# Optimization experiments

Hardware: AMD Instinct MI355X
Metric: run time of the kernel (lower is better)

## Reference

```python
import jax, jax.numpy as jnp
import numpy as np

B, N, C, O, K, D = 32, 2048, 64, 64, 3, 16

def setup_inputs() -> dict:
    key = jax.random.key(0)
    ks = jax.random.split(key, 6)
    x = jax.random.normal(ks[0], (B, N, C), dtype=jnp.float32)
    node_embeddings = jax.random.normal(ks[1], (N, D), dtype=jnp.float32)
    adj_m = jax.random.uniform(ks[2], (N, N), dtype=jnp.float32)
    weights_pool = jax.random.normal(ks[3], (D, K, C, O), dtype=jnp.float32) * 0.1
    bias_pool = jax.random.normal(ks[4], (D, O), dtype=jnp.float32) * 0.1
    sa_weight = jax.random.normal(ks[5], (N, 2 * N), dtype=jnp.float32) * (1.0 / np.sqrt(2 * N))
    return {"x": x, "node_embeddings": node_embeddings, "adj_m": adj_m,
            "weights_pool": weights_pool, "bias_pool": bias_pool, "sa_weight": sa_weight}

def reference(x, node_embeddings, adj_m, weights_pool, bias_pool, sa_weight):
    n = node_embeddings.shape[0]
    # learned adaptive adjacency [N,N]
    supports = jax.nn.softmax(jax.nn.relu(node_embeddings @ node_embeddings.T), axis=1)
    # SpatialAttention: 1x1 conv over 2N channels == matmul with [N,2N] weight
    z = jnp.concatenate([supports, adj_m], axis=1) @ sa_weight.T  # [N,N]
    s2 = jax.nn.sigmoid(z)
    supports = s2 * adj_m + (1.0 - s2) * supports
    # Chebyshev polynomial basis
    support_set = [jnp.eye(n, dtype=supports.dtype), supports]
    for _ in range(2, K):
        support_set.append(2.0 * supports @ support_set[-1] - support_set[-2])
    supports_k = jnp.stack(support_set, axis=0)  # [K,N,N]
    # per-node generated weights/bias from embeddings
    weights = jnp.einsum('nd,dkio->nkio', node_embeddings, weights_pool)  # [N,K,C,O]
    bias = node_embeddings @ bias_pool  # [N,O]
    # graph conv: aggregate then per-node matmul
    x_g = jnp.einsum('knm,bmc->bnkc', supports_k, x)  # [B,N,K,C]
    x_gconv = jnp.einsum('bnki,nkio->bno', x_g, weights) + bias  # [B,N,O]
    return x_gconv
```

## Files before the change

### kernel.cpp

```cpp
#include <hip/hip_runtime.h>


typedef unsigned short u16;
typedef float f32x4 __attribute__((ext_vector_type(4)));
typedef __bf16 bf16x8 __attribute__((ext_vector_type(8)));
typedef unsigned short u16x8 __attribute__((ext_vector_type(8)));

#define PSTRIDE ((size_t)2048 * 2048)

__device__ __forceinline__ u16 f2bf(float f) {
    unsigned u = __float_as_uint(f);
    u += 0x7FFFu + ((u >> 16) & 1u);
    return (u16)(u >> 16);
}
__device__ __forceinline__ float bf2f(u16 h) {
    return __uint_as_float((unsigned)h << 16);
}
__device__ __forceinline__ void gl_lds16(const void* g, void* l) {
    __builtin_amdgcn_global_load_lds(
        (const __attribute__((address_space(1))) unsigned*)g,
        (__attribute__((address_space(3))) unsigned*)l, 16, 0, 0);
}

__global__ __launch_bounds__(256)
void preamble(const float* __restrict__ E, const float* __restrict__ adj,
              const float* __restrict__ saw, const float* __restrict__ x,
              const float* __restrict__ Wp, const float* __restrict__ bp,
              float* __restrict__ zf, u16* __restrict__ Acat,
              u16* __restrict__ sawb, u16* __restrict__ xtT,
              u16* __restrict__ Wpb, float* __restrict__ Wpbf,
              float* __restrict__ bias, u16* __restrict__ xn, int mode) {
    __shared__ u16 t[64][65];
    __shared__ float Bp[1024];
    const int bid = blockIdx.x, tid = threadIdx.x;

    if (bid < 256) {
        const int c0 = (bid & 31) * 64, r0 = (bid >> 5) * 256;
        const int r = r0 + tid;
        const float4* Er = (const float4*)(E + (size_t)r * 16);
        float4 e0 = Er[0], e1 = Er[1], e2 = Er[2], e3 = Er[3];
        *(float4*)(Bp + tid * 4) = *(const float4*)(E + (size_t)c0 * 16 + tid * 4);
        __syncthreads();
        float* zr = zf + (size_t)r * 2048 + c0;
#pragma unroll
        for (int cc = 0; cc < 4; ++cc) {
            float acc[16];
#pragma unroll
            for (int c = 0; c < 16; ++c) {
                const float* bp2 = Bp + (cc * 16 + c) * 16;
                float s = 0.f;
                s = fmaf(e0.x, bp2[0], s);  s = fmaf(e0.y, bp2[1], s);
                s = fmaf(e0.z, bp2[2], s);  s = fmaf(e0.w, bp2[3], s);
                s = fmaf(e1.x, bp2[4], s);  s = fmaf(e1.y, bp2[5], s);
                s = fmaf(e1.z, bp2[6], s);  s = fmaf(e1.w, bp2[7], s);
                s = fmaf(e2.x, bp2[8], s);  s = fmaf(e2.y, bp2[9], s);
                s = fmaf(e2.z, bp2[10], s); s = fmaf(e2.w, bp2[11], s);
                s = fmaf(e3.x, bp2[12], s); s = fmaf(e3.y, bp2[13], s);
                s = fmaf(e3.z, bp2[14], s); s = fmaf(e3.w, bp2[15], s);
                acc[c] = fmaxf(s, 0.f);
            }
#pragma unroll
            for (int q = 0; q < 4; ++q)
                *(float4*)(zr + cc * 16 + q * 4) =
                    make_float4(acc[q * 4], acc[q * 4 + 1], acc[q * 4 + 2], acc[q * 4 + 3]);
        }
    } else if (bid < 4352) {
        size_t j = ((size_t)(bid - 256) * 256 + tid) * 4;
        float4 v = *(const float4*)(adj + j);
        int n = (int)(j >> 11), c = (int)(j & 2047);
        ushort4 o = make_ushort4(f2bf(v.x), f2bf(v.y), f2bf(v.z), f2bf(v.w));
        *(ushort4*)(Acat + (size_t)n * 4096 + 2048 + c) = o;
    } else if (bid < 12544) {
        size_t j = ((size_t)(bid - 4352) * 256 + tid) * 4;
        float4 v = *(const float4*)(saw + j);
        ushort4 o = make_ushort4(f2bf(v.x), f2bf(v.y), f2bf(v.z), f2bf(v.w));
        *(ushort4*)(sawb + j) = o;
    } else if (bid < 13568) {
        int local = bid - 12544;
        int m0 = (local & 31) * 64, b = local >> 5;
        int c = tid & 63, g = tid >> 6;
#pragma unroll
        for (int r = 0; r < 16; ++r) {
            int mm = g * 16 + r;
            t[mm][c] = f2bf(x[((size_t)b * 2048 + m0 + mm) * 64 + c]);
        }
        __syncthreads();
#pragma unroll
        for (int r = 0; r < 16; ++r) {
            int cc = g * 16 + r;
            xtT[((size_t)b * 64 + cc) * 2048 + m0 + c] = t[c][cc];
        }
        if (mode) {
#pragma unroll
            for (int r = 0; r < 16; ++r) {
                int mm = g * 16 + r;
                xn[((size_t)(m0 + mm)) * 2048 + b * 64 + c] = t[mm][c];
            }
        }
    } else {
        int local = bid - 13568;
        if (local < 16) {
            const int d = local;
            const float* base = Wp + (size_t)d * 12288;
            for (int idx = tid; idx < 12288; idx += 256) {
                int o = idx / 192, ki = idx - o * 192;
                int k = ki >> 6, i = ki & 63;
                float v;
                if (k == 0)      v = base[i * 64 + o] - base[2 * 4096 + i * 64 + o];
                else if (k == 1) v = base[4096 + i * 64 + o];
                else             v = 2.f * base[2 * 4096 + i * 64 + o];
                size_t dst = (size_t)(d * 64 + o) * 192 + ki;
                Wpb[dst] = f2bf(v);
                Wpbf[dst] = v;
            }
        } else {
            const int nb = local - 16;
#pragma unroll
            for (int it = 0; it < 8; ++it) {
                int idx = tid + it * 256;
                int n = nb * 32 + (idx >> 6), o = idx & 63;
                float s = 0.f;
#pragma unroll
                for (int d = 0; d < 16; ++d) s = fmaf(E[n * 16 + d], bp[d * 64 + o], s);
                bias[(size_t)n * 64 + o] = s;
            }
        }
    }
}

__global__ __launch_bounds__(256)
void mid(const float* __restrict__ zf, u16* __restrict__ Acat,
         const float* __restrict__ E, const float* __restrict__ Wpbf,
         u16* __restrict__ Wnb) {
    __shared__ float red[4];
    __shared__ float Es[32 * 16];
    const int bid = blockIdx.x, tid = threadIdx.x;
    if (bid < 2048) {
        const int n = bid, lane = tid & 63, wave = tid >> 6;
        const float* zr = zf + (size_t)n * 2048;
        float4 a = *(const float4*)(zr + tid * 8);
        float4 b = *(const float4*)(zr + tid * 8 + 4);
        float mx = fmaxf(fmaxf(fmaxf(a.x, a.y), fmaxf(a.z, a.w)),
                         fmaxf(fmaxf(b.x, b.y), fmaxf(b.z, b.w)));
        for (int off = 32; off; off >>= 1) mx = fmaxf(mx, __shfl_down(mx, off, 64));
        if (lane == 0) red[wave] = mx;
        __syncthreads();
        mx = fmaxf(fmaxf(red[0], red[1]), fmaxf(red[2], red[3]));
        __syncthreads();
        float v[8] = {__expf(a.x - mx), __expf(a.y - mx), __expf(a.z - mx), __expf(a.w - mx),
                      __expf(b.x - mx), __expf(b.y - mx), __expf(b.z - mx), __expf(b.w - mx)};
        float sum = v[0] + v[1] + v[2] + v[3] + v[4] + v[5] + v[6] + v[7];
        for (int off = 32; off; off >>= 1) sum += __shfl_down(sum, off, 64);
        if (lane == 0) red[wave] = sum;
        __syncthreads();
        sum = red[0] + red[1] + red[2] + red[3];
        float inv = 1.f / sum;
        u16* orow = Acat + (size_t)n * 4096 + tid * 8;
        *(ushort4*)orow = make_ushort4(f2bf(v[0] * inv), f2bf(v[1] * inv),
                                       f2bf(v[2] * inv), f2bf(v[3] * inv));
        *(ushort4*)(orow + 4) = make_ushort4(f2bf(v[4] * inv), f2bf(v[5] * inv),
                                             f2bf(v[6] * inv), f2bf(v[7] * inv));
    } else {
        const int w = bid - 2048;
        const int c0 = (w % 12) * 1024, n0 = (w / 12) * 32;
        for (int j = tid; j < 512; j += 256) Es[j] = E[(size_t)n0 * 16 + j];
        float4 wf[16];
#pragma unroll
        for (int d = 0; d < 16; ++d)
            wf[d] = *(const float4*)(Wpbf + (size_t)d * 12288 + c0 + tid * 4);
        __syncthreads();
        for (int nl = 0; nl < 32; ++nl) {
            float4 s = make_float4(0.f, 0.f, 0.f, 0.f);
#pragma unroll
            for (int d = 0; d < 16; ++d) {
                float e = Es[nl * 16 + d];
                s.x = fmaf(e, wf[d].x, s.x);
                s.y = fmaf(e, wf[d].y, s.y);
                s.z = fmaf(e, wf[d].z, s.z);
                s.w = fmaf(e, wf[d].w, s.w);
            }
            *(ushort4*)(Wnb + (size_t)(n0 + nl) * 12288 + c0 + tid * 4) =
                make_ushort4(f2bf(s.x), f2bf(s.y), f2bf(s.z), f2bf(s.w));
        }
    }
}

__global__ __launch_bounds__(256, 3)
void gemm_bt(const u16* __restrict__ A, const u16* __restrict__ Bt,
             u16* __restrict__ Cp, int M, int N, int K, int Kh) {
    __shared__ alignas(16) u16 As[128 * 64];
    __shared__ alignas(16) u16 Bs[128 * 64];
    const int tid = threadIdx.x, lane = tid & 63, wave = tid >> 6;
    const int m0 = blockIdx.y * 128, n0 = blockIdx.x * 128;
    const int wm = (wave >> 1) * 64, wn = (wave & 1) * 64;
    const int kbeg = blockIdx.z * Kh, kend = kbeg + Kh;
    const int ml = lane & 15, c0l = lane >> 4;
    f32x4 acc[4][4] = {};

    int sIdx[4], rowI[4], gcI[4];
#pragma unroll
    for (int r = 0; r < 4; ++r) {
        int s = wave * 64 + r * 256 + lane;
        sIdx[r] = s; rowI[r] = s >> 3; gcI[r] = (s & 7) ^ ((s >> 3) & 7);
    }
    int baseA[4], mskA[4], baseB[4], mskB[4];
#pragma unroll
    for (int i = 0; i < 4; ++i) { int m = wm + i * 16 + ml; baseA[i] = m * 8; mskA[i] = m & 7; }
#pragma unroll
    for (int j = 0; j < 4; ++j) { int nn = wn + j * 16 + ml; baseB[j] = nn * 8; mskB[j] = nn & 7; }

    u16x8 ra[4], rb[4];
#pragma unroll
    for (int r = 0; r < 4; ++r) {
        ra[r] = *(const u16x8*)(A + (size_t)(m0 + rowI[r]) * K + kbeg + gcI[r] * 8);
        rb[r] = *(const u16x8*)(Bt + (size_t)(n0 + rowI[r]) * K + kbeg + gcI[r] * 8);
    }
#pragma unroll
    for (int r = 0; r < 4; ++r) {
        *(u16x8*)(As + (size_t)sIdx[r] * 8) = ra[r];
        *(u16x8*)(Bs + (size_t)sIdx[r] * 8) = rb[r];
    }
    __syncthreads();

    for (int k0 = kbeg; k0 < kend; k0 += 64) {
        const bool more = (k0 + 64) < kend;
        if (more) {
#pragma unroll
            for (int r = 0; r < 4; ++r) {
                ra[r] = *(const u16x8*)(A + (size_t)(m0 + rowI[r]) * K + (k0 + 64) + gcI[r] * 8);
                rb[r] = *(const u16x8*)(Bt + (size_t)(n0 + rowI[r]) * K + (k0 + 64) + gcI[r] * 8);
            }
        }
#pragma unroll
        for (int ks4 = 0; ks4 < 8; ks4 += 4) {
            bf16x8 af[4], bv[4];
#pragma unroll
            for (int i = 0; i < 4; ++i)
                af[i] = *(const bf16x8*)(As + (baseA[i] + ((c0l + ks4) ^ mskA[i])) * 8);
#pragma unroll
            for (int j = 0; j < 4; ++j)
                bv[j] = *(const bf16x8*)(Bs + (baseB[j] + ((c0l + ks4) ^ mskB[j])) * 8);
#pragma unroll
            for (int i = 0; i < 4; ++i)
#pragma unroll
                for (int j = 0; j < 4; ++j)
                    acc[i][j] = __builtin_amdgcn_mfma_f32_16x16x32_bf16(af[i], bv[j], acc[i][j], 0, 0, 0);
        }
        if (more) {
            __syncthreads();
#pragma unroll
            for (int r = 0; r < 4; ++r) {
                *(u16x8*)(As + (size_t)sIdx[r] * 8) = ra[r];
                *(u16x8*)(Bs + (size_t)sIdx[r] * 8) = rb[r];
            }
            __syncthreads();
        }
    }

    const int col_l = lane & 15, row_l = (lane >> 4) * 4;
    u16* Cz = Cp + (size_t)blockIdx.z * M * N;
#pragma unroll
    for (int i = 0; i < 4; ++i)
#pragma unroll
        for (int j = 0; j < 4; ++j)
#pragma unroll
            for (int r = 0; r < 4; ++r) {
                int row = m0 + wm + i * 16 + row_l + r;
                int col = n0 + wn + j * 16 + col_l;
                Cz[(size_t)row * N + col] = f2bf(acc[i][j][r]);
            }
}

__global__ __launch_bounds__(256)
void reduce_z(const u16* __restrict__ p, const u16* __restrict__ Acat,
              u16* __restrict__ S) {
    size_t j = ((size_t)blockIdx.x * 256 + threadIdx.x) * 4;
    ushort4 p0 = *(const ushort4*)(p + j);
    ushort4 p1 = *(const ushort4*)(p + PSTRIDE + j);
    ushort4 p2 = *(const ushort4*)(p + 2 * PSTRIDE + j);
    ushort4 p3 = *(const ushort4*)(p + 3 * PSTRIDE + j);
    int row = (int)(j >> 11), col = (int)(j & 2047);
    ushort4 sp = *(const ushort4*)(Acat + (size_t)row * 4096 + col);
    ushort4 ad = *(const ushort4*)(Acat + (size_t)row * 4096 + 2048 + col);
    float z0 = bf2f(p0.x) + bf2f(p1.x) + bf2f(p2.x) + bf2f(p3.x);
    float z1 = bf2f(p0.y) + bf2f(p1.y) + bf2f(p2.y) + bf2f(p3.y);
    float z2 = bf2f(p0.z) + bf2f(p1.z) + bf2f(p2.z) + bf2f(p3.z);
    float z3 = bf2f(p0.w) + bf2f(p1.w) + bf2f(p2.w) + bf2f(p3.w);
    float s0 = 1.f / (1.f + __expf(-z0)), s1 = 1.f / (1.f + __expf(-z1));
    float s2 = 1.f / (1.f + __expf(-z2)), s3 = 1.f / (1.f + __expf(-z3));
    ushort4 o = make_ushort4(
        f2bf(s0 * bf2f(ad.x) + (1.f - s0) * bf2f(sp.x)),
        f2bf(s1 * bf2f(ad.y) + (1.f - s1) * bf2f(sp.y)),
        f2bf(s2 * bf2f(ad.z) + (1.f - s2) * bf2f(sp.z)),
        f2bf(s3 * bf2f(ad.w) + (1.f - s3) * bf2f(sp.w)));
    *(ushort4*)(S + j) = o;
}

__global__ __launch_bounds__(256)
void reduceT(const u16* __restrict__ p, u16* __restrict__ xg1o,
             u16* __restrict__ xg1T, int mode) {
    __shared__ u16 t[64][68];
    int bx = blockIdx.x * 64, by = blockIdx.y * 64;
    int cg = threadIdx.x & 15, rg = threadIdx.x >> 4;
    int b = bx >> 6;
#pragma unroll
    for (int rr = 0; rr < 4; ++rr) {
        int row = rg * 4 + rr;
        size_t idx = (size_t)(by + row) * 2048 + bx + cg * 4;
        ushort4 q0 = *(const ushort4*)(p + idx);
        ushort4 q1 = *(const ushort4*)(p + PSTRIDE + idx);
        ushort4 q2 = *(const ushort4*)(p + 2 * PSTRIDE + idx);
        ushort4 q3 = *(const ushort4*)(p + 3 * PSTRIDE + idx);
        ushort4 v = make_ushort4(
            f2bf(bf2f(q0.x) + bf2f(q1.x) + bf2f(q2.x) + bf2f(q3.x)),
            f2bf(bf2f(q0.y) + bf2f(q1.y) + bf2f(q2.y) + bf2f(q3.y)),
            f2bf(bf2f(q0.z) + bf2f(q1.z) + bf2f(q2.z) + bf2f(q3.z)),
            f2bf(bf2f(q0.w) + bf2f(q1.w) + bf2f(q2.w) + bf2f(q3.w)));
        if (mode) *(ushort4*)(xg1o + idx) = v;
        else      *(ushort4*)(xg1o + ((size_t)b * 2048 + by + row) * 64 + cg * 4) = v;
        *(ushort4*)(&t[row][cg * 4]) = v;
    }
    __syncthreads();
    int c = threadIdx.x & 63, g = threadIdx.x >> 6;
#pragma unroll
    for (int r = 0; r < 16; ++r) {
        int row = g * 16 + r;
        xg1T[(size_t)(bx + row) * 2048 + by + c] = t[c][row];
    }
}

__global__ __launch_bounds__(256, 4)
void gconv_wn(const u16* __restrict__ xn, const u16* __restrict__ xg1n,
              const u16* __restrict__ p, const u16* __restrict__ Wnb,
              const float* __restrict__ bias, float* __restrict__ out) {
    __shared__ alignas(16) u16 As[32 * 192];
    __shared__ alignas(16) u16 Bs[64 * 192];
    const int n = blockIdx.x, tid = threadIdx.x;
    const int lane = tid & 63, wave = tid >> 6;
    const int wn2 = wave * 16;
    const int ml = lane & 15, c0l = lane >> 4;
    const int col = lane & 15, rl = (lane >> 4) * 4;

#pragma unroll
    for (int it = 0; it < 6; ++it) {
        int s = tid + it * 256;
        int row = s / 24, sc = s - row * 24;
        int gc = (sc & 24) | ((sc ^ row) & 7);
        gl_lds16(Wnb + (size_t)n * 12288 + (size_t)row * 192 + gc * 8, Bs + (size_t)s * 8);
    }
#pragma unroll
    for (int it = 0; it < 3; ++it) {
        int s = tid + it * 256;
        int row = s / 24, sc = s - row * 24;
        int gc = (sc & 24) | ((sc ^ row) & 7);
        u16x8 v;
        if (gc < 8) {
            v = *(const u16x8*)(xn + (size_t)n * 2048 + row * 64 + (gc & 7) * 8);
        } else if (gc < 16) {
            v = *(const u16x8*)(xg1n + (size_t)n * 2048 + row * 64 + (gc & 7) * 8);
        } else {
            const u16* pp = p + (size_t)n * 2048 + row * 64 + (gc & 7) * 8;
            u16x8 q0 = *(const u16x8*)pp;
            u16x8 q1 = *(const u16x8*)(pp + PSTRIDE);
            u16x8 q2 = *(const u16x8*)(pp + 2 * PSTRIDE);
            u16x8 q3 = *(const u16x8*)(pp + 3 * PSTRIDE);
#pragma unroll
            for (int tt = 0; tt < 8; ++tt)
                v[tt] = f2bf(bf2f(q0[tt]) + bf2f(q1[tt]) + bf2f(q2[tt]) + bf2f(q3[tt]));
        }
        *(u16x8*)(As + (size_t)s * 8) = v;
    }
    float bv0 = bias[(size_t)n * 64 + wn2 + col];
    f32x4 acc[2];
#pragma unroll
    for (int mt = 0; mt < 2; ++mt)
#pragma unroll
        for (int r = 0; r < 4; ++r) acc[mt][r] = bv0;
    __syncthreads();

#pragma unroll
    for (int ks = 0; ks < 6; ++ks) {
        int c = c0l + ks * 4;
        int o = wn2 + ml;
        bf16x8 bfrag = *(const bf16x8*)(Bs + (o * 24 + ((c & 24) | ((c ^ (o & 7)) & 7))) * 8);
#pragma unroll
        for (int mt = 0; mt < 2; ++mt) {
            int m = mt * 16 + ml;
            bf16x8 afrag = *(const bf16x8*)(As + (m * 24 + ((c & 24) | ((c ^ (m & 7)) & 7))) * 8);
            acc[mt] = __builtin_amdgcn_mfma_f32_16x16x32_bf16(afrag, bfrag, acc[mt], 0, 0, 0);
        }
    }
#pragma unroll
    for (int mt = 0; mt < 2; ++mt)
#pragma unroll
        for (int r = 0; r < 4; ++r) {
            int b = mt * 16 + rl + r;
            out[((size_t)b * 2048 + n) * 64 + wn2 + col] = acc[mt][r];
        }
}

__global__ __launch_bounds__(256, 2)
void gconv_mfma(const float* __restrict__ x, const u16* __restrict__ xg1,
                const u16* __restrict__ p, const u16* __restrict__ Wpb,
                const float* __restrict__ bias, const float* __restrict__ E,
                float* __restrict__ out) {
    __shared__ alignas(16) float El[16 * 128];
    const int tid = threadIdx.x, lane = tid & 63, wave = tid >> 6;
    const int m0 = blockIdx.x * 128, nb = m0 & 2047, bB = m0 >> 11;
    const int wm = (wave >> 1) * 64, wn = (wave & 1) * 32;
    const int ml = lane & 15, c0l = lane >> 4;
    const int col_l = lane & 15, rl = (lane >> 4) * 4;

#pragma unroll
    for (int it = 0; it < 8; ++it) {
        int idx = tid + it * 256;
        El[idx] = E[(size_t)(nb + (idx & 127)) * 16 + (idx >> 7)];
    }
    __syncthreads();

    bf16x8 af[4][6];
#pragma unroll
    for (int i = 0; i < 4; ++i) {
        const int row = m0 + wm + i * 16 + ml;
        const int n = row & 2047;
#pragma unroll
        for (int ks = 0; ks < 2; ++ks) {
            const float* xp = x + (size_t)row * 64 + (c0l + ks * 4) * 8;
            float4 a = *(const float4*)xp, b4 = *(const float4*)(xp + 4);
            u16x8 v;
            v[0] = f2bf(a.x);  v[1] = f2bf(a.y);  v[2] = f2bf(a.z);  v[3] = f2bf(a.w);
            v[4] = f2bf(b4.x); v[5] = f2bf(b4.y); v[6] = f2bf(b4.z); v[7] = f2bf(b4.w);
            af[i][ks] = __builtin_bit_cast(bf16x8, v);
        }
#pragma unroll
        for (int ks = 2; ks < 4; ++ks)
            af[i][ks] = *(const bf16x8*)(xg1 + (size_t)row * 64 + (c0l + ks * 4 - 8) * 8);
#pragma unroll
        for (int ks = 4; ks < 6; ++ks) {
            const u16* pp = p + (size_t)n * 2048 + bB * 64 + (c0l + ks * 4 - 16) * 8;
            u16x8 q0 = *(const u16x8*)pp;
            u16x8 q1 = *(const u16x8*)(pp + PSTRIDE);
            u16x8 q2 = *(const u16x8*)(pp + 2 * PSTRIDE);
            u16x8 q3 = *(const u16x8*)(pp + 3 * PSTRIDE);
            u16x8 v;
#pragma unroll
            for (int tt = 0; tt < 8; ++tt)
                v[tt] = f2bf(bf2f(q0[tt]) + bf2f(q1[tt]) + bf2f(q2[tt]) + bf2f(q3[tt]));
            af[i][ks] = __builtin_bit_cast(bf16x8, v);
        }
    }

    f32x4 oacc[4][2];
#pragma unroll
    for (int i = 0; i < 4; ++i)
#pragma unroll
        for (int j = 0; j < 2; ++j)
#pragma unroll
            for (int r = 0; r < 4; ++r)
                oacc[i][j][r] = bias[(size_t)(nb + wm + i * 16 + rl + r) * 64 + wn + j * 16 + col_l];

#pragma unroll 2
    for (int d = 0; d < 16; ++d) {
        bf16x8 bv[2][6];
#pragma unroll
        for (int j = 0; j < 2; ++j) {
            const u16* wp = Wpb + (size_t)(d * 64 + wn + j * 16 + ml) * 192 + c0l * 8;
#pragma unroll
            for (int ks = 0; ks < 6; ++ks)
                bv[j][ks] = *(const bf16x8*)(wp + ks * 32);
        }
        f32x4 tmp[4][2] = {};
#pragma unroll
        for (int ks = 0; ks < 6; ++ks)
#pragma unroll
            for (int i = 0; i < 4; ++i)
#pragma unroll
                for (int j = 0; j < 2; ++j)
                    tmp[i][j] = __builtin_amdgcn_mfma_f32_16x16x32_bf16(af[i][ks], bv[j][ks], tmp[i][j], 0, 0, 0);
#pragma unroll
        for (int i = 0; i < 4; ++i) {
            f32x4 ev = *(const f32x4*)(El + d * 128 + wm + i * 16 + rl);
#pragma unroll
            for (int r = 0; r < 4; ++r)
#pragma unroll
                for (int j = 0; j < 2; ++j)
                    oacc[i][j][r] = fmaf(ev[r], tmp[i][j][r], oacc[i][j][r]);
        }
    }
#pragma unroll
    for (int i = 0; i < 4; ++i)
#pragma unroll
        for (int j = 0; j < 2; ++j)
#pragma unroll
            for (int r = 0; r < 4; ++r)
                out[(size_t)(m0 + wm + i * 16 + rl + r) * 64 + wn + j * 16 + col_l] = oacc[i][j][r];
}

extern "C" void kernel_launch(void* const* d_in, const int* in_sizes, int n_in,
                              void* d_out, int out_size, void* d_ws, size_t ws_size,
                              hipStream_t stream) {
    const float* x   = (const float*)d_in[0];
    const float* E   = (const float*)d_in[1];
    const float* adj = (const float*)d_in[2];
    const float* Wp  = (const float*)d_in[3];
    const float* bp  = (const float*)d_in[4];
    const float* saw = (const float*)d_in[5];
    float* out = (float*)d_out;

    char* ws = (char*)d_ws;
    const size_t MB = 1u << 20;
    const int wn_mode = (ws_size >= 140 * MB) ? 1 : 0;

    u16*   Acat  = (u16*)(ws);
    u16*   sawb  = (u16*)(ws + 16 * MB);
    u16*   XtT   = (u16*)(ws + 32 * MB);
    u16*   Wpb   = (u16*)(ws + 40 * MB);
    float* bias  = (float*)(ws + 41 * MB);
    float* Wpbf  = (float*)(ws + 42 * MB);
    float* zf    = (float*)(ws + 48 * MB);
    u16*   part  = (u16*)(ws + 48 * MB);
    u16*   S_bf  = (u16*)(ws + 16 * MB);
    u16*   xg1T  = (u16*)(ws + 24 * MB);
    u16*   xg1o  = (u16*)(ws);
    u16*   xn    = (u16*)(ws + 80 * MB);
    u16*   Wnb   = (u16*)(ws + 88 * MB);

    preamble<<<13648, 256, 0, stream>>>(E, adj, saw, x, Wp, bp, zf, Acat, sawb, XtT,
                                        Wpb, Wpbf, bias, xn, wn_mode);
    mid<<<wn_mode ? 2816 : 2048, 256, 0, stream>>>(zf, Acat, E, Wpbf, Wnb);

    gemm_bt<<<dim3(16, 16, 4), 256, 0, stream>>>(Acat, sawb, part, 2048, 2048, 4096, 1024);
    reduce_z<<<4096, 256, 0, stream>>>(part, Acat, S_bf);
    gemm_bt<<<dim3(16, 16, 4), 256, 0, stream>>>(S_bf, XtT, part, 2048, 2048, 2048, 512);
    reduceT<<<dim3(32, 32), 256, 0, stream>>>(part, xg1o, xg1T, wn_mode);
    gemm_bt<<<dim3(16, 16, 4), 256, 0, stream>>>(S_bf, xg1T, part, 2048, 2048, 2048, 512);

    if (wn_mode)
        gconv_wn<<<2048, 256, 0, stream>>>(xn, xg1o, part, Wnb, bias, out);
    else
        gconv_mfma<<<512, 256, 0, stream>>>(x, xg1o, part, Wpb, bias, E, out);
}
```

Before: 278.6 us.

## Replace GEMM with 256x256 tile, double-buffered direct-to-LDS loads and XCD remap

The bf16 MFMA GEMM moves from 128x128 tiles with 256 threads to 256x256 tiles with 512 threads and 8 waves. Global data now goes straight into LDS through global_load_lds into a double buffer, so the next K-slice loads while the current one is computed. MFMA bursts are split into four quadrant phases with barriers and s_setprio, and workgroup IDs are remapped so blocks spread across XCDs. Each GEMM now launches only 256 workgroups with 128KB of LDS per block, which may underfill the GPU's 256 CUs and limits how many blocks fit per CU.

```diff
diff --git a/kernel.cpp b/kernel.cpp
--- a/kernel.cpp
+++ b/kernel.cpp
@@ -185,87 +185,162 @@
     }
 }
 
-__global__ __launch_bounds__(256, 3)
-void gemm_bt(const u16* __restrict__ A, const u16* __restrict__ Bt,
-             u16* __restrict__ Cp, int M, int N, int K, int Kh) {
-    __shared__ alignas(16) u16 As[128 * 64];
-    __shared__ alignas(16) u16 Bs[128 * 64];
+__global__ __launch_bounds__(512, 2)
+void gemm_bt256(const u16* __restrict__ A, const u16* __restrict__ Bt,
+                u16* __restrict__ Cp, int M, int N, int K, int Kh) {
+    __shared__ alignas(16) u16 As[2][256 * 64];
+    __shared__ alignas(16) u16 Bs[2][256 * 64];
     const int tid = threadIdx.x, lane = tid & 63, wave = tid >> 6;
-    const int m0 = blockIdx.y * 128, n0 = blockIdx.x * 128;
-    const int wm = (wave >> 1) * 64, wn = (wave & 1) * 64;
-    const int kbeg = blockIdx.z * Kh, kend = kbeg + Kh;
+
+    const int nbx = gridDim.x, nby = gridDim.y, nbz = gridDim.z;
+    const int nwg = nbx * nby * nbz;
+    int lin = (blockIdx.z * nby + blockIdx.y) * nbx + blockIdx.x;
+    if ((nwg & 7) == 0) lin = (lin & 7) * (nwg >> 3) + (lin >> 3);
+    const int bz = lin / (nbx * nby);
+    const int r2 = lin - bz * nbx * nby;
+    const int by = r2 / nbx, bx = r2 - by * nbx;
+
+    const int m0 = by * 256, n0 = bx * 256;
+    const int kbeg = bz * Kh;
+    const int NT = Kh >> 6;
+    const int wm = (wave >> 2) * 128, wn = (wave & 3) * 64;
     const int ml = lane & 15, c0l = lane >> 4;
-    f32x4 acc[4][4] = {};
-
-    int sIdx[4], rowI[4], gcI[4];
+
+    int sI[4], rowI[4], gcI[4];
 #pragma unroll
     for (int r = 0; r < 4; ++r) {
-        int s = wave * 64 + r * 256 + lane;
-        sIdx[r] = s; rowI[r] = s >> 3; gcI[r] = (s & 7) ^ ((s >> 3) & 7);
-    }
-    int baseA[4], mskA[4], baseB[4], mskB[4];
-#pragma unroll
-    for (int i = 0; i < 4; ++i) { int m = wm + i * 16 + ml; baseA[i] = m * 8; mskA[i] = m & 7; }
-#pragma unroll
-    for (int j = 0; j < 4; ++j) { int nn = wn + j * 16 + ml; baseB[j] = nn * 8; mskB[j] = nn & 7; }
-
-    u16x8 ra[4], rb[4];
-#pragma unroll
-    for (int r = 0; r < 4; ++r) {
-        ra[r] = *(const u16x8*)(A + (size_t)(m0 + rowI[r]) * K + kbeg + gcI[r] * 8);
-        rb[r] = *(const u16x8*)(Bt + (size_t)(n0 + rowI[r]) * K + kbeg + gcI[r] * 8);
-    }
-#pragma unroll
-    for (int r = 0; r < 4; ++r) {
-        *(u16x8*)(As + (size_t)sIdx[r] * 8) = ra[r];
-        *(u16x8*)(Bs + (size_t)sIdx[r] * 8) = rb[r];
-    }
-    __syncthreads();
-
-    for (int k0 = kbeg; k0 < kend; k0 += 64) {
-        const bool more = (k0 + 64) < kend;
-        if (more) {
+        int s = r * 512 + tid;
+        sI[r] = s; rowI[r] = s >> 3; gcI[r] = (s & 7) ^ ((s >> 3) & 7);
+    }
+
+    f32x4 acc[8][4] = {};
+
+#pragma unroll
+    for (int r = 0; r < 4; ++r)
+        gl_lds16(A + (size_t)(m0 + rowI[r]) * K + kbeg + gcI[r] * 8, &As[0][sI[r] * 8]);
+#pragma unroll
+    for (int r = 0; r < 4; ++r)
+        gl_lds16(Bt + (size_t)(n0 + rowI[r]) * K + kbeg + gcI[r] * 8, &Bs[0][sI[r] * 8]);
+    asm volatile("s_waitcnt vmcnt(0)" ::: "memory");
+    __builtin_amdgcn_s_barrier();
+
+    for (int t = 0; t < NT; ++t) {
+        const int cur = t & 1;
+        const u16* Asc = As[cur];
+        const u16* Bsc = Bs[cur];
+
+        if (t + 1 < NT) {
+            const int k1 = kbeg + (t + 1) * 64;
+            u16* Ad = (u16*)As[cur ^ 1];
+            u16* Bd = (u16*)Bs[cur ^ 1];
+#pragma unroll
+            for (int r = 0; r < 4; ++r)
+                gl_lds16(A + (size_t)(m0 + rowI[r]) * K + k1 + gcI[r] * 8, Ad + sI[r] * 8);
+#pragma unroll
+            for (int r = 0; r < 4; ++r)
+                gl_lds16(Bt + (size_t)(n0 + rowI[r]) * K + k1 + gcI[r] * 8, Bd + sI[r] * 8);
+        }
+
+        bf16x8 af[4][2], bv[2][2];
+
+#pragma unroll
+        for (int i = 0; i < 4; ++i) {
+            const int mr = wm + i * 16 + ml;
+#pragma unroll
+            for (int ks = 0; ks < 2; ++ks)
+                af[i][ks] = *(const bf16x8*)(Asc + mr * 64 + (((c0l + ks * 4) ^ (mr & 7)) * 8));
+        }
+#pragma unroll
+        for (int j = 0; j < 2; ++j) {
+            const int nr = wn + j * 16 + ml;
+#pragma unroll
+            for (int ks = 0; ks < 2; ++ks)
+                bv[j][ks] = *(const bf16x8*)(Bsc + nr * 64 + (((c0l + ks * 4) ^ (nr & 7)) * 8));
+        }
+        __builtin_amdgcn_s_barrier();
+        asm volatile("s_waitcnt lgkmcnt(0)" ::: "memory");
+        __builtin_amdgcn_s_setprio(1);
+#pragma unroll
+        for (int ks = 0; ks < 2; ++ks)
+#pragma unroll
+            for (int i = 0; i < 4; ++i)
+#pragma unroll
+                for (int j = 0; j < 2; ++j)
+                    acc[i][j] = __builtin_amdgcn_mfma_f32_16x16x32_bf16(af[i][ks], bv[j][ks], acc[i][j], 0, 0, 0);
+        __builtin_amdgcn_s_setprio(0);
+        __builtin_amdgcn_s_barrier();
+
+#pragma unroll
+        for (int j = 0; j < 2; ++j) {
+            const int nr = wn + (2 + j) * 16 + ml;
+#pragma unroll
+            for (int ks = 0; ks < 2; ++ks)
+                bv[j][ks] = *(const bf16x8*)(Bsc + nr * 64 + (((c0l + ks * 4) ^ (nr & 7)) * 8));
+        }
+        __builtin_amdgcn_s_barrier();
+        asm volatile("s_waitcnt lgkmcnt(0)" ::: "memory");
+        __builtin_amdgcn_s_setprio(1);
+#pragma unroll
+        for (int ks = 0; ks < 2; ++ks)
+#pragma unroll
+            for (int i = 0; i < 4; ++i)
+#pragma unroll
+                for (int j = 0; j < 2; ++j)
+                    acc[i][2 + j] = __builtin_amdgcn_mfma_f32_16x16x32_bf16(af[i][ks], bv[j][ks], acc[i][2 + j], 0, 0, 0);
+        __builtin_amdgcn_s_setprio(0);
+        __builtin_amdgcn_s_barrier();
+
+#pragma unroll
+        for (int i = 0; i < 4; ++i) {
+            const int mr = wm + (4 + i) * 16 + ml;
+#pragma unroll
+            for (int ks = 0; ks < 2; ++ks)
+                af[i][ks] = *(const bf16x8*)(Asc + mr * 64 + (((c0l + ks * 4) ^ (mr & 7)) * 8));
+        }
+        __builtin_amdgcn_s_barrier();
+        asm volatile("s_waitcnt lgkmcnt(0)" ::: "memory");
+        __builtin_amdgcn_s_setprio(1);
+#pragma unroll
+        for (int ks = 0; ks < 2; ++ks)
+#pragma unroll
+            for (int i = 0; i < 4; ++i)
+#pragma unroll
+                for (int j = 0; j < 2; ++j)
+                    acc[4 + i][2 + j] = __builtin_amdgcn_mfma_f32_16x16x32_bf16(af[i][ks], bv[j][ks], acc[4 + i][2 + j], 0, 0, 0);
+        __builtin_amdgcn_s_setprio(0);
+        __builtin_amdgcn_s_barrier();
+
+#pragma unroll
+        for (int j = 0; j < 2; ++j) {
+            const int nr = wn + j * 16 + ml;
+#pragma unroll
+            for (int ks = 0; ks < 2; ++ks)
+                bv[j][ks] = *(const bf16x8*)(Bsc + nr * 64 + (((c0l + ks * 4) ^ (nr & 7)) * 8));
+        }
+        __builtin_amdgcn_s_barrier();
+        asm volatile("s_waitcnt lgkmcnt(0)" ::: "memory");
+        __builtin_amdgcn_s_setprio(1);
+#pragma unroll
+        for (int ks = 0; ks < 2; ++ks)
+#pragma unroll
+            for (int i = 0; i < 4; ++i)
+#pragma unroll
+                for (int j = 0; j < 2; ++j)
+                    acc[4 + i][j] = __builtin_amdgcn_mfma_f32_16x16x32_bf16(af[i][ks], bv[j][ks], acc[4 + i][j], 0, 0, 0);
+        __builtin_amdgcn_s_setprio(0);
+        asm volatile("s_waitcnt vmcnt(0)" ::: "memory");
+        __builtin_amdgcn_s_barrier();
+    }
+
+    const int col_l = lane & 15, rl = (lane >> 4) * 4;
+    u16* Cz = Cp + (size_t)bz * M * N;
+#pragma unroll
+    for (int i = 0; i < 8; ++i)
+#pragma unroll
+        for (int j = 0; j < 4; ++j)
 #pragma unroll
             for (int r = 0; r < 4; ++r) {
-                ra[r] = *(const u16x8*)(A + (size_t)(m0 + rowI[r]) * K + (k0 + 64) + gcI[r] * 8);
-                rb[r] = *(const u16x8*)(Bt + (size_t)(n0 + rowI[r]) * K + (k0 + 64) + gcI[r] * 8);
-            }
-        }
-#pragma unroll
-        for (int ks4 = 0; ks4 < 8; ks4 += 4) {
-            bf16x8 af[4], bv[4];
-#pragma unroll
-            for (int i = 0; i < 4; ++i)
-                af[i] = *(const bf16x8*)(As + (baseA[i] + ((c0l + ks4) ^ mskA[i])) * 8);
-#pragma unroll
-            for (int j = 0; j < 4; ++j)
-                bv[j] = *(const bf16x8*)(Bs + (baseB[j] + ((c0l + ks4) ^ mskB[j])) * 8);
-#pragma unroll
-            for (int i = 0; i < 4; ++i)
-#pragma unroll
-                for (int j = 0; j < 4; ++j)
-                    acc[i][j] = __builtin_amdgcn_mfma_f32_16x16x32_bf16(af[i], bv[j], acc[i][j], 0, 0, 0);
-        }
-        if (more) {
-            __syncthreads();
-#pragma unroll
-            for (int r = 0; r < 4; ++r) {
-                *(u16x8*)(As + (size_t)sIdx[r] * 8) = ra[r];
-                *(u16x8*)(Bs + (size_t)sIdx[r] * 8) = rb[r];
-            }
-            __syncthreads();
-        }
-    }
-
-    const int col_l = lane & 15, row_l = (lane >> 4) * 4;
-    u16* Cz = Cp + (size_t)blockIdx.z * M * N;
-#pragma unroll
-    for (int i = 0; i < 4; ++i)
-#pragma unroll
-        for (int j = 0; j < 4; ++j)
-#pragma unroll
-            for (int r = 0; r < 4; ++r) {
-                int row = m0 + wm + i * 16 + row_l + r;
+                int row = m0 + wm + i * 16 + rl + r;
                 int col = n0 + wn + j * 16 + col_l;
                 Cz[(size_t)row * N + col] = f2bf(acc[i][j][r]);
             }
@@ -529,11 +604,11 @@
                                         Wpb, Wpbf, bias, xn, wn_mode);
     mid<<<wn_mode ? 2816 : 2048, 256, 0, stream>>>(zf, Acat, E, Wpbf, Wnb);
 
-    gemm_bt<<<dim3(16, 16, 4), 256, 0, stream>>>(Acat, sawb, part, 2048, 2048, 4096, 1024);
+    gemm_bt256<<<dim3(8, 8, 4), 512, 0, stream>>>(Acat, sawb, part, 2048, 2048, 4096, 1024);
     reduce_z<<<4096, 256, 0, stream>>>(part, Acat, S_bf);
-    gemm_bt<<<dim3(16, 16, 4), 256, 0, stream>>>(S_bf, XtT, part, 2048, 2048, 2048, 512);
+    gemm_bt256<<<dim3(8, 8, 4), 512, 0, stream>>>(S_bf, XtT, part, 2048, 2048, 2048, 512);
     reduceT<<<dim3(32, 32), 256, 0, stream>>>(part, xg1o, xg1T, wn_mode);
-    gemm_bt<<<dim3(16, 16, 4), 256, 0, stream>>>(S_bf, xg1T, part, 2048, 2048, 2048, 512);
+    gemm_bt256<<<dim3(8, 8, 4), 512, 0, stream>>>(S_bf, xg1T, part, 2048, 2048, 2048, 512);
 
     if (wn_mode)
         gconv_wn<<<2048, 256, 0, stream>>>(xn, xg1o, part, Wnb, bias, out);
```

New measurement: 292.4 us. 5.0% more time.
